# Performance work log

Measured on AMD Instinct MI355X. Metric: run time of the kernel, lower is better.

## Reference

```python
import jax, jax.numpy as jnp
import numpy as np

LAMBDA_DEPTHG = 0.3
STEGO_TEMPERATURE = 0.1
KNN_K = 7
DEPTH_SIGMA = 0.5
EPS = 1e-8


def _l2norm(x):
    return x / jnp.sqrt(jnp.sum(x * x, axis=-1, keepdims=True) + EPS)


def _stego_loss(codes, feats, temperature, knn_k):
    # Pairwise cosine similarity of DINO features -> KNN graph (includes self).
    f = _l2norm(feats)                                  # (B,N,Df)
    sim_f = jnp.einsum('bnd,bmd->bnm', f, f)            # (B,N,N)
    _, knn_idx = jax.lax.top_k(sim_f, knn_k)            # (B,N,k) int32
    # Temperature-scaled InfoNCE over code similarities; KNN entries are positives.
    c = _l2norm(codes)                                  # (B,N,Dc)
    logits = jnp.einsum('bnd,bmd->bnm', c, c) / temperature  # (B,N,N)
    logp = jax.nn.log_softmax(logits, axis=-1)          # (B,N,N)
    pos_logp = jnp.take_along_axis(logp, knn_idx, axis=-1)   # (B,N,k)
    return -jnp.mean(pos_logp)


def _depth_guided_correlation_loss(codes, depth, sigma_d):
    # Gaussian depth affinity: pixels at similar depth should have similar codes.
    dd = depth[:, :, None] - depth[:, None, :]          # (B,N,N)
    w = jnp.exp(-(dd * dd) / (2.0 * sigma_d * sigma_d)) # (B,N,N)
    c = _l2norm(codes)
    s = jnp.einsum('bnd,bmd->bnm', c, c)                # (B,N,N) cosine corr
    return jnp.mean(w * (1.0 - s))


def setup_inputs() -> dict:
    key = jax.random.key(0)
    k1, k2, k3 = jax.random.split(key, 3)
    B, N = 2, 4096
    semantic_codes = jax.random.normal(k1, (B, N, 90), dtype=jnp.float32)
    dino_features = jax.random.normal(k2, (B, N, 384), dtype=jnp.float32)
    depth = jax.random.uniform(k3, (B, N), dtype=jnp.float32)
    return {"semantic_codes": semantic_codes, "dino_features": dino_features, "depth": depth}


def reference(semantic_codes, dino_features, depth):
    l_stego = _stego_loss(semantic_codes, dino_features, STEGO_TEMPERATURE, KNN_K)
    l_depthg = _depth_guided_correlation_loss(semantic_codes, depth, DEPTH_SIGMA)
    total = l_stego + LAMBDA_DEPTHG * l_depthg
    return (l_stego, l_depthg, total)
```

## Files before the change

kernel.cpp:

```cpp
#include <hip/hip_runtime.h>
#include <math.h>

#define NPTS 4096

typedef __attribute__((ext_vector_type(8))) short bf16x8;
typedef __attribute__((ext_vector_type(16))) float f32x16;

#define KEEP(x) asm volatile("" : "+v"(x))

__device__ __forceinline__ f32x16 zero16() {
  f32x16 z;
#pragma unroll
  for (int i = 0; i < 16; ++i) z[i] = 0.f;
  return z;
}

__device__ __forceinline__ unsigned packkey(float x, int m) {
  unsigned u = __float_as_uint(x);
  unsigned key = u ^ ((unsigned)((int)u >> 31) | 0x80000000u);
  return (key & 0xFFFFF000u) | (unsigned)m;
}

__device__ __forceinline__ void cas7(unsigned v, unsigned* s) {
#pragma unroll
  for (int t = 0; t < 7; ++t) {
    const unsigned hi = s[t] >= v ? s[t] : v;
    const unsigned lo = s[t] >= v ? v : s[t];
    s[t] = hi;
    v = lo;
  }
}

__device__ __forceinline__ unsigned bf16pack(float a, float b) {
  unsigned ua = __float_as_uint(a); ua = (ua + 0x7FFFu + ((ua >> 16) & 1u)) >> 16;
  unsigned ub = __float_as_uint(b); ub = (ub + 0x7FFFu + ((ub >> 16) & 1u)) >> 16;
  return ua | (ub << 16);
}

__global__ __launch_bounds__(64) void norm_f(const float* __restrict__ feats,
                                             unsigned short* __restrict__ Fsw) {
  const int row = blockIdx.x;
  const int lane = threadIdx.x;
  const int b = row >> 12, mt = (row >> 5) & 127, rl = row & 31;

  const float* f = feats + (size_t)row * 384;
  float v[8];
  float ss = 0.f;
  if (lane < 48) {
    float4 p0 = *(const float4*)(f + lane * 8);
    float4 p1 = *(const float4*)(f + lane * 8 + 4);
    v[0] = p0.x; v[1] = p0.y; v[2] = p0.z; v[3] = p0.w;
    v[4] = p1.x; v[5] = p1.y; v[6] = p1.z; v[7] = p1.w;
#pragma unroll
    for (int e = 0; e < 8; ++e) ss = fmaf(v[e], v[e], ss);
  }
#pragma unroll
  for (int m = 1; m <= 32; m <<= 1) ss += __shfl_xor(ss, m, 64);
  const float inv = rsqrtf(ss + 1e-8f);
  if (lane < 48) {
    uint4 o;
    o.x = bf16pack(v[0] * inv, v[1] * inv);
    o.y = bf16pack(v[2] * inv, v[3] * inv);
    o.z = bf16pack(v[4] * inv, v[5] * inv);
    o.w = bf16pack(v[6] * inv, v[7] * inv);
    const int kc = lane >> 1, hs = lane & 1;
    *(uint4*)(Fsw + (((size_t)(b * 128 + mt) * 24 + kc) << 9) + (hs * 32 + rl) * 8) = o;
  }
}

__global__ __launch_bounds__(64) void norm_c(const float* __restrict__ codes,
                                             unsigned short* __restrict__ Csw,
                                             float* __restrict__ invc) {
  const int row = blockIdx.x;
  const int lane = threadIdx.x;
  const int b = row >> 12, mt = (row >> 5) & 127, rl = row & 31;

  const float* c = codes + (size_t)row * 90;
  float cv[8];
#pragma unroll
  for (int e = 0; e < 8; ++e) cv[e] = 0.f;
  if (lane < 11) {
    float4 p0 = *(const float4*)(c + lane * 8);
    float4 p1 = *(const float4*)(c + lane * 8 + 4);
    cv[0] = p0.x; cv[1] = p0.y; cv[2] = p0.z; cv[3] = p0.w;
    cv[4] = p1.x; cv[5] = p1.y; cv[6] = p1.z; cv[7] = p1.w;
  } else if (lane == 11) {
    cv[0] = c[88]; cv[1] = c[89];
  }
  float cs = 0.f;
#pragma unroll
  for (int e = 0; e < 8; ++e) cs = fmaf(cv[e], cv[e], cs);
#pragma unroll
  for (int m = 1; m <= 32; m <<= 1) cs += __shfl_xor(cs, m, 64);
  const float cinv = rsqrtf(cs + 1e-8f);
  if (lane < 12) {
    uint4 o;
    o.x = bf16pack(cv[0] * cinv, cv[1] * cinv);
    o.y = bf16pack(cv[2] * cinv, cv[3] * cinv);
    o.z = bf16pack(cv[4] * cinv, cv[5] * cinv);
    o.w = bf16pack(cv[6] * cinv, cv[7] * cinv);
    const int kc = lane >> 1, hs = lane & 1;
    *(uint4*)(Csw + (((size_t)(b * 128 + mt) * 6 + kc) << 9) + (hs * 32 + rl) * 8) = o;
  }
  if (lane == 0) invc[row] = cinv;
}

__global__ __launch_bounds__(256, 1) void knn_mfma(const unsigned short* __restrict__ Fsw,
                                                   unsigned* __restrict__ cand) {
  __shared__ unsigned ckey[4][32][7];
  const int g = blockIdx.x;
  const int b = g & 1;
  const int p = (g >> 1) & 3;
  const int qt = g >> 3;
  const int q0 = qt * 32;
  const int tid = threadIdx.x;
  const int w = tid >> 6;
  const int lane = tid & 63;
  const int lo = lane & 31, hi4 = (lane >> 5) * 4;
  const unsigned short* Fb = Fsw + (size_t)b * 128 * 24 * 512;

  bf16x8 bfr[24];
  {
    const unsigned short* qb = Fb + ((size_t)qt * 24) * 512 + lane * 8;
#pragma unroll
    for (int t = 0; t < 24; ++t) bfr[t] = *(const bf16x8*)(qb + t * 512);
#pragma unroll
    for (int t = 0; t < 24; ++t) KEEP(bfr[t]);
  }
  unsigned s7[7];
#pragma unroll
  for (int t = 0; t < 7; ++t) s7[t] = 0u;

  const int t0 = p * 32 + w * 8;
  const unsigned short* ab = Fb + ((size_t)t0 * 24) * 512 + lane * 8;

  bf16x8 a0[12], a1[12];
#pragma unroll
  for (int t = 0; t < 12; ++t) a0[t] = *(const bf16x8*)(ab + t * 512);
#pragma unroll
  for (int t = 0; t < 12; ++t) KEEP(a0[t]);

  for (int mt = 0; mt < 8; ++mt) {
    const unsigned short* art = ab + (size_t)mt * 24 * 512;
#pragma unroll
    for (int t = 0; t < 12; ++t) a1[t] = *(const bf16x8*)(art + (12 + t) * 512);
#pragma unroll
    for (int t = 0; t < 12; ++t) KEEP(a1[t]);
    f32x16 acc = zero16();
#pragma unroll
    for (int t = 0; t < 12; ++t)
      acc = __builtin_amdgcn_mfma_f32_32x32x16_bf16(a0[t], bfr[t], acc, 0, 0, 0);
    if (mt + 1 < 8) {
      const unsigned short* arn = ab + (size_t)(mt + 1) * 24 * 512;
#pragma unroll
      for (int t = 0; t < 12; ++t) a0[t] = *(const bf16x8*)(arn + t * 512);
#pragma unroll
      for (int t = 0; t < 12; ++t) KEEP(a0[t]);
    }
#pragma unroll
    for (int t = 0; t < 12; ++t)
      acc = __builtin_amdgcn_mfma_f32_32x32x16_bf16(a1[t], bfr[12 + t], acc, 0, 0, 0);
    const int mb = (t0 + mt) * 32 + hi4;
#pragma unroll
    for (int r = 0; r < 16; ++r) {
      const int m = mb + (r & 3) + 8 * (r >> 2);
      cas7(packkey(acc[r], m), s7);
    }
  }

#pragma unroll
  for (int t = 0; t < 7; ++t) {
    const unsigned ov = (unsigned)__shfl_xor((int)s7[t], 32, 64);
    cas7(ov, s7);
  }
  if (lane < 32) {
#pragma unroll
    for (int t = 0; t < 7; ++t) ckey[w][lo][t] = s7[t];
  }
  __syncthreads();

  if (tid < 32) {
    unsigned fs[7];
#pragma unroll
    for (int t = 0; t < 7; ++t) fs[t] = 0u;
    for (int w2 = 0; w2 < 4; ++w2)
#pragma unroll
      for (int t = 0; t < 7; ++t) cas7(ckey[w2][tid][t], fs);
    unsigned* o = cand + ((size_t)((p * 2 + b) * NPTS) + q0 + tid) * 7;
#pragma unroll
    for (int t = 0; t < 7; ++t) o[t] = fs[t];
  }
}

__global__ __launch_bounds__(256, 1) void lse_depth(const unsigned short* __restrict__ Csw,
                                                    const float* __restrict__ depth,
                                                    float* __restrict__ slse_part,
                                                    float* __restrict__ dpart) {
  __shared__ float lsep[4][32];
  __shared__ float depp[4];
  const int g = blockIdx.x;
  const int b = g & 1;
  const int p = (g >> 1) & 3;
  const int qt = g >> 3;
  const int q0 = qt * 32;
  const int tid = threadIdx.x;
  const int w = tid >> 6;
  const int lane = tid & 63;
  const int lo = lane & 31, hi4 = (lane >> 5) * 4;
  const unsigned short* Cb = Csw + (size_t)b * 128 * 6 * 512;
  const float* db = depth + b * NPTS;

  bf16x8 bfr[6];
  {
    const unsigned short* qb = Cb + ((size_t)qt * 6) * 512 + lane * 8;
#pragma unroll
    for (int t = 0; t < 6; ++t) bfr[t] = *(const bf16x8*)(qb + t * 512);
#pragma unroll
    for (int t = 0; t < 6; ++t) KEEP(bfr[t]);
  }
  const float dq = db[q0 + lo];
  float slse = 0.f, sdep = 0.f;

  const int t0 = p * 32 + w * 8;
  const unsigned short* ab = Cb + ((size_t)t0 * 6) * 512 + lane * 8;

  bf16x8 a0[6], a1[6];
#pragma unroll
  for (int t = 0; t < 6; ++t) a0[t] = *(const bf16x8*)(ab + t * 512);
#pragma unroll
  for (int t = 0; t < 6; ++t) KEEP(a0[t]);

#define PROC3(A, GT)                                                           \
  {                                                                            \
    f32x16 acc = zero16();                                                     \
    _Pragma("unroll")                                                          \
    for (int t = 0; t < 6; ++t)                                                \
      acc = __builtin_amdgcn_mfma_f32_32x32x16_bf16(A[t], bfr[t], acc, 0, 0, 0); \
    float dvv[16];                                                             \
    _Pragma("unroll")                                                          \
    for (int k = 0; k < 4; ++k) {                                              \
      float4 dv = *(const float4*)(db + (GT) * 32 + hi4 + 8 * k);              \
      dvv[k * 4 + 0] = dv.x; dvv[k * 4 + 1] = dv.y;                            \
      dvv[k * 4 + 2] = dv.z; dvv[k * 4 + 3] = dv.w;                            \
    }                                                                          \
    _Pragma("unroll")                                                          \
    for (int r = 0; r < 16; ++r) {                                             \
      const float s = acc[r];                                                  \
      const float dd = dq - dvv[r];                                            \
      sdep += __expf(-2.f * dd * dd) * (1.f - s);                              \
      slse += __expf(fmaf(s, 10.f, -10.f));                                    \
    }                                                                          \
  }

  for (int mt = 0; mt < 8; mt += 2) {
    {
      const unsigned short* ar = ab + (size_t)(mt + 1) * 6 * 512;
#pragma unroll
      for (int t = 0; t < 6; ++t) a1[t] = *(const bf16x8*)(ar + t * 512);
#pragma unroll
      for (int t = 0; t < 6; ++t) KEEP(a1[t]);
    }
    PROC3(a0, t0 + mt)
    if (mt + 2 < 8) {
      const unsigned short* ar = ab + (size_t)(mt + 2) * 6 * 512;
#pragma unroll
      for (int t = 0; t < 6; ++t) a0[t] = *(const bf16x8*)(ar + t * 512);
#pragma unroll
      for (int t = 0; t < 6; ++t) KEEP(a0[t]);
    }
    PROC3(a1, t0 + mt + 1)
  }
#undef PROC3

  slse += __shfl_xor(slse, 32, 64);
  if (lane < 32) lsep[w][lo] = slse;
#pragma unroll
  for (int m = 1; m <= 32; m <<= 1) sdep += __shfl_xor(sdep, m, 64);
  if (lane == 0) depp[w] = sdep;
  __syncthreads();
  if (tid < 32) {
    float tot = 0.f;
#pragma unroll
    for (int w2 = 0; w2 < 4; ++w2) tot += lsep[w2][tid];
    slse_part[(size_t)((p * 2 + b) * NPTS) + q0 + tid] = tot;
  }
  if (tid == 32) {
    float d = 0.f;
#pragma unroll
    for (int w2 = 0; w2 < 4; ++w2) d += depp[w2];
    dpart[g] = d;
  }
}

__global__ __launch_bounds__(64) void gather_pos(const float* __restrict__ codes,
                                                 const float* __restrict__ invc,
                                                 const unsigned* __restrict__ cand,
                                                 float* __restrict__ gpart) {
  const int n = blockIdx.x;
  const int b = n >> 12, q = n & 4095;
  const int lane = threadIdx.x;

  unsigned s[7];
#pragma unroll
  for (int t = 0; t < 7; ++t) s[t] = 0u;
#pragma unroll
  for (int pp = 0; pp < 4; ++pp) {
    const unsigned* cp = cand + ((size_t)((pp * 2 + b) * NPTS) + q) * 7;
#pragma unroll
    for (int t = 0; t < 7; ++t) cas7(cp[t], s);
  }
  bool has = false;
#pragma unroll
  for (int t = 0; t < 7; ++t) has = has || ((s[t] & 4095u) == (unsigned)q);
  if (!has) s[6] = (unsigned)q;

  const float* cn = codes + (size_t)n * 90;
  float2 a = make_float2(0.f, 0.f);
  if (lane < 45) a = *(const float2*)(cn + lane * 2);
  const float inva = invc[n];
  float ssum = 0.f;
#pragma unroll
  for (int k = 0; k < 7; ++k) {
    const int m = (int)(s[k] & 4095u);
    const float* cm = codes + ((size_t)(b << 12) + m) * 90;
    float2 bb = make_float2(0.f, 0.f);
    if (lane < 45) bb = *(const float2*)(cm + lane * 2);
    float p = fmaf(a.x, bb.x, a.y * bb.y);
#pragma unroll
    for (int w = 1; w <= 32; w <<= 1) p += __shfl_xor(p, w, 64);
    ssum += p * inva * invc[(b << 12) + m];
  }
  if (lane == 0) gpart[n] = ssum;
}

__global__ __launch_bounds__(256) void finalize(const float* __restrict__ slse_part,
                                                const float* __restrict__ gpart,
                                                const float* __restrict__ dpart,
                                                float* __restrict__ out) {
  const int tid = threadIdx.x;
  float s1 = 0.f, s2 = 0.f;
  for (int n = tid; n < 2 * NPTS; n += 256) {
    const int b = n >> 12, q = n & 4095;
    float pz = 0.f;
#pragma unroll
    for (int pp = 0; pp < 4; ++pp) pz += slse_part[(pp * 2 + b) * NPTS + q];
    s1 += 10.f + __logf(pz);
    s2 += gpart[n];
  }
  float s3 = 0.f;
#pragma unroll
  for (int k = 0; k < 4; ++k) s3 += dpart[tid + k * 256];
  __shared__ float r1[256], r2[256], r3[256];
  r1[tid] = s1; r2[tid] = s2; r3[tid] = s3;
  __syncthreads();
  for (int s = 128; s > 0; s >>= 1) {
    if (tid < s) { r1[tid] += r1[tid + s]; r2[tid] += r2[tid + s]; r3[tid] += r3[tid + s]; }
    __syncthreads();
  }
  if (tid == 0) {
    const float l_st = (7.f * r1[0] - 10.f * r2[0]) / 57344.f;
    const float l_dp = r3[0] / 33554432.f;
    out[0] = l_st;
    out[1] = l_dp;
    out[2] = l_st + 0.3f * l_dp;
  }
}

extern "C" void kernel_launch(void* const* d_in, const int* in_sizes, int n_in,
                              void* d_out, int out_size, void* d_ws, size_t ws_size,
                              hipStream_t stream) {
  (void)in_sizes; (void)n_in; (void)out_size; (void)ws_size;
  const float* codes = (const float*)d_in[0];
  const float* feats = (const float*)d_in[1];
  const float* depth = (const float*)d_in[2];
  float* out = (float*)d_out;

  char* ws = (char*)d_ws;
  float*    invc      = (float*)ws;
  unsigned* cand      = (unsigned*)(ws + 32768);
  unsigned short* Fsw = (unsigned short*)(ws + 950272);
  unsigned short* Csw = (unsigned short*)(ws + 950272);
  float*    slse_part = (float*)(ws + 2523136);
  float*    dpart     = (float*)(ws + 2654208);
  float*    gpart     = (float*)(ws + 2658304);

  norm_f<<<2 * NPTS, 64, 0, stream>>>(feats, Fsw);
  knn_mfma<<<1024, 256, 0, stream>>>(Fsw, cand);
  norm_c<<<2 * NPTS, 64, 0, stream>>>(codes, Csw, invc);
  lse_depth<<<1024, 256, 0, stream>>>(Csw, depth, slse_part, dpart);
  gather_pos<<<2 * NPTS, 64, 0, stream>>>(codes, invc, cand, gpart);
  finalize<<<1, 256, 0, stream>>>(slse_part, gpart, dpart, out);
}
```

Before: 101.8 us.

## Pipeline top-k epilogue with next tile MFMAs and skip insertions below threshold

The KNN candidate kernel now double-buffers accumulators, so the top-7 insertion for the previous 32x32 tile is interleaved with the MFMA chain of the current tile. Each candidate insertion is also gated by a wave-wide check against the current 7th-best key, which skips most of the sorting-network work. The sentinel initial key changes to a small finite value so the threshold can be unpacked as a float. This adds a wave vote per element and relies on divergence-free branches, and it raises register pressure from the second accumulator.

```diff
diff --git a/kernel.cpp b/kernel.cpp
--- a/kernel.cpp
+++ b/kernel.cpp
@@ -19,6 +19,11 @@
   unsigned u = __float_as_uint(x);
   unsigned key = u ^ ((unsigned)((int)u >> 31) | 0x80000000u);
   return (key & 0xFFFFF000u) | (unsigned)m;
+}
+
+__device__ __forceinline__ float unpackkey(unsigned key) {
+  const unsigned m1 = (unsigned)((int)key >> 31);
+  return __uint_as_float(key ^ ((~m1) | 0x80000000u));
 }
 
 __device__ __forceinline__ void cas7(unsigned v, unsigned* s) {
@@ -30,6 +35,8 @@
     v = lo;
   }
 }
+
+#define KSENT 0x00800000u
 
 __device__ __forceinline__ unsigned bf16pack(float a, float b) {
   unsigned ua = __float_as_uint(a); ua = (ua + 0x7FFFu + ((ua >> 16) & 1u)) >> 16;
@@ -129,44 +136,66 @@
   }
   unsigned s7[7];
 #pragma unroll
-  for (int t = 0; t < 7; ++t) s7[t] = 0u;
+  for (int t = 0; t < 7; ++t) s7[t] = KSENT;
 
   const int t0 = p * 32 + w * 8;
   const unsigned short* ab = Fb + ((size_t)t0 * 24) * 512 + lane * 8;
 
   bf16x8 a0[12], a1[12];
-#pragma unroll
-  for (int t = 0; t < 12; ++t) a0[t] = *(const bf16x8*)(ab + t * 512);
-#pragma unroll
-  for (int t = 0; t < 12; ++t) KEEP(a0[t]);
-
-  for (int mt = 0; mt < 8; ++mt) {
-    const unsigned short* art = ab + (size_t)mt * 24 * 512;
-#pragma unroll
-    for (int t = 0; t < 12; ++t) a1[t] = *(const bf16x8*)(art + (12 + t) * 512);
-#pragma unroll
-    for (int t = 0; t < 12; ++t) KEEP(a1[t]);
-    f32x16 acc = zero16();
-#pragma unroll
-    for (int t = 0; t < 12; ++t)
-      acc = __builtin_amdgcn_mfma_f32_32x32x16_bf16(a0[t], bfr[t], acc, 0, 0, 0);
-    if (mt + 1 < 8) {
-      const unsigned short* arn = ab + (size_t)(mt + 1) * 24 * 512;
-#pragma unroll
-      for (int t = 0; t < 12; ++t) a0[t] = *(const bf16x8*)(arn + t * 512);
-#pragma unroll
-      for (int t = 0; t < 12; ++t) KEEP(a0[t]);
-    }
-#pragma unroll
-    for (int t = 0; t < 12; ++t)
-      acc = __builtin_amdgcn_mfma_f32_32x32x16_bf16(a1[t], bfr[12 + t], acc, 0, 0, 0);
-    const int mb = (t0 + mt) * 32 + hi4;
-#pragma unroll
-    for (int r = 0; r < 16; ++r) {
-      const int m = mb + (r & 3) + 8 * (r >> 2);
-      cas7(packkey(acc[r], m), s7);
-    }
-  }
+
+#define LOADA0(MT)                                                             \
+  { const unsigned short* ar_ = ab + (size_t)(MT) * 24 * 512;                  \
+    _Pragma("unroll")                                                          \
+    for (int t = 0; t < 12; ++t) a0[t] = *(const bf16x8*)(ar_ + t * 512);      \
+    _Pragma("unroll")                                                          \
+    for (int t = 0; t < 12; ++t) KEEP(a0[t]); }
+
+#define LOADA1(MT)                                                             \
+  { const unsigned short* ar_ = ab + (size_t)(MT) * 24 * 512;                  \
+    _Pragma("unroll")                                                          \
+    for (int t = 0; t < 12; ++t) a1[t] = *(const bf16x8*)(ar_ + (12 + t) * 512); \
+    _Pragma("unroll")                                                          \
+    for (int t = 0; t < 12; ++t) KEEP(a1[t]); }
+
+#define EPI8(ACC, MT, R0)                                                      \
+  { const float thr_ = unpackkey(s7[6]);                                       \
+    const int mb_ = (t0 + (MT)) * 32 + hi4;                                    \
+    _Pragma("unroll")                                                          \
+    for (int r = (R0); r < (R0) + 8; ++r) {                                    \
+      const float v_ = ACC[r];                                                 \
+      if (__any(v_ > thr_))                                                    \
+        cas7(packkey(v_, mb_ + (r & 3) + 8 * (r >> 2)), s7);                   \
+    } }
+
+#define TILE(ACC, MT, PACC, PMT, DOEPI)                                        \
+  LOADA1(MT)                                                                   \
+  ACC = zero16();                                                              \
+  _Pragma("unroll")                                                            \
+  for (int t = 0; t < 12; ++t)                                                 \
+    ACC = __builtin_amdgcn_mfma_f32_32x32x16_bf16(a0[t], bfr[t], ACC, 0, 0, 0); \
+  if (DOEPI) { EPI8(PACC, PMT, 0) }                                            \
+  if ((MT) + 1 < 8) { LOADA0((MT) + 1) }                                       \
+  _Pragma("unroll")                                                            \
+  for (int t = 0; t < 12; ++t)                                                 \
+    ACC = __builtin_amdgcn_mfma_f32_32x32x16_bf16(a1[t], bfr[12 + t], ACC, 0, 0, 0); \
+  if (DOEPI) { EPI8(PACC, PMT, 8) }
+
+  LOADA0(0)
+  f32x16 accA, accB;
+  TILE(accA, 0, accB, 0, 0)
+  TILE(accB, 1, accA, 0, 1)
+  TILE(accA, 2, accB, 1, 1)
+  TILE(accB, 3, accA, 2, 1)
+  TILE(accA, 4, accB, 3, 1)
+  TILE(accB, 5, accA, 4, 1)
+  TILE(accA, 6, accB, 5, 1)
+  TILE(accB, 7, accA, 6, 1)
+  EPI8(accB, 7, 0)
+  EPI8(accB, 7, 8)
+#undef TILE
+#undef EPI8
+#undef LOADA0
+#undef LOADA1
 
 #pragma unroll
   for (int t = 0; t < 7; ++t) {
@@ -182,7 +211,7 @@
   if (tid < 32) {
     unsigned fs[7];
 #pragma unroll
-    for (int t = 0; t < 7; ++t) fs[t] = 0u;
+    for (int t = 0; t < 7; ++t) fs[t] = KSENT;
     for (int w2 = 0; w2 < 4; ++w2)
 #pragma unroll
       for (int t = 0; t < 7; ++t) cas7(ckey[w2][tid][t], fs);
@@ -302,7 +331,7 @@
 
   unsigned s[7];
 #pragma unroll
-  for (int t = 0; t < 7; ++t) s[t] = 0u;
+  for (int t = 0; t < 7; ++t) s[t] = KSENT;
 #pragma unroll
   for (int pp = 0; pp < 4; ++pp) {
     const unsigned* cp = cand + ((size_t)((pp * 2 + b) * NPTS) + q) * 7;
```

Result: slower. 130.2 us (+27.9%).

## Use FP8 MFMA for KNN similarity and widen lse_depth blocks to 512 threads

Applied to the files above, without the earlier changes.

Normalized DINO features are now stored as FP8 (scaled by 8) instead of bf16, and the KNN similarity GEMM uses the fp8 32x32x16 MFMA. This halves the feature bytes loaded and uses a higher-throughput MFMA path. The cost is lower precision in the similarity values, which could change which neighbours top-k selects. Separately, lse_depth switches to 512 blocks of 512 threads, so the workspace keeps two partial sums instead of four and finalize reduces fewer partials.

```diff
diff --git a/kernel.cpp b/kernel.cpp
--- a/kernel.cpp
+++ b/kernel.cpp
@@ -5,6 +5,7 @@
 
 typedef __attribute__((ext_vector_type(8))) short bf16x8;
 typedef __attribute__((ext_vector_type(16))) float f32x16;
+typedef long fp8x8;
 
 #define KEEP(x) asm volatile("" : "+v"(x))
 
@@ -31,6 +32,8 @@
   }
 }
 
+#define KSENT 0u
+
 __device__ __forceinline__ unsigned bf16pack(float a, float b) {
   unsigned ua = __float_as_uint(a); ua = (ua + 0x7FFFu + ((ua >> 16) & 1u)) >> 16;
   unsigned ub = __float_as_uint(b); ub = (ub + 0x7FFFu + ((ub >> 16) & 1u)) >> 16;
@@ -38,7 +41,7 @@
 }
 
 __global__ __launch_bounds__(64) void norm_f(const float* __restrict__ feats,
-                                             unsigned short* __restrict__ Fsw) {
+                                             unsigned char* __restrict__ Fsw8) {
   const int row = blockIdx.x;
   const int lane = threadIdx.x;
   const int b = row >> 12, mt = (row >> 5) & 127, rl = row & 31;
@@ -56,15 +59,15 @@
   }
 #pragma unroll
   for (int m = 1; m <= 32; m <<= 1) ss += __shfl_xor(ss, m, 64);
-  const float inv = rsqrtf(ss + 1e-8f);
+  const float s8 = rsqrtf(ss + 1e-8f) * 8.0f;
   if (lane < 48) {
-    uint4 o;
-    o.x = bf16pack(v[0] * inv, v[1] * inv);
-    o.y = bf16pack(v[2] * inv, v[3] * inv);
-    o.z = bf16pack(v[4] * inv, v[5] * inv);
-    o.w = bf16pack(v[6] * inv, v[7] * inv);
+    int w0 = __builtin_amdgcn_cvt_pk_fp8_f32(v[0] * s8, v[1] * s8, 0, 0);
+    w0 = __builtin_amdgcn_cvt_pk_fp8_f32(v[2] * s8, v[3] * s8, w0, 1);
+    int w1 = __builtin_amdgcn_cvt_pk_fp8_f32(v[4] * s8, v[5] * s8, 0, 0);
+    w1 = __builtin_amdgcn_cvt_pk_fp8_f32(v[6] * s8, v[7] * s8, w1, 1);
     const int kc = lane >> 1, hs = lane & 1;
-    *(uint4*)(Fsw + (((size_t)(b * 128 + mt) * 24 + kc) << 9) + (hs * 32 + rl) * 8) = o;
+    uint2 o = make_uint2((unsigned)w0, (unsigned)w1);
+    *(uint2*)(Fsw8 + (((size_t)(b * 128 + mt) * 24 + kc) << 9) + (hs * 32 + rl) * 8) = o;
   }
 }
 
@@ -105,7 +108,7 @@
   if (lane == 0) invc[row] = cinv;
 }
 
-__global__ __launch_bounds__(256, 1) void knn_mfma(const unsigned short* __restrict__ Fsw,
+__global__ __launch_bounds__(256, 1) void knn_mfma(const unsigned char* __restrict__ Fsw8,
                                                    unsigned* __restrict__ cand) {
   __shared__ unsigned ckey[4][32][7];
   const int g = blockIdx.x;
@@ -117,49 +120,49 @@
   const int w = tid >> 6;
   const int lane = tid & 63;
   const int lo = lane & 31, hi4 = (lane >> 5) * 4;
-  const unsigned short* Fb = Fsw + (size_t)b * 128 * 24 * 512;
-
-  bf16x8 bfr[24];
+  const unsigned char* Fb = Fsw8 + (size_t)b * 128 * 24 * 512;
+
+  fp8x8 bfr[24];
   {
-    const unsigned short* qb = Fb + ((size_t)qt * 24) * 512 + lane * 8;
-#pragma unroll
-    for (int t = 0; t < 24; ++t) bfr[t] = *(const bf16x8*)(qb + t * 512);
+    const unsigned char* qb = Fb + ((size_t)qt * 24) * 512 + lane * 8;
+#pragma unroll
+    for (int t = 0; t < 24; ++t) bfr[t] = *(const fp8x8*)(qb + t * 512);
 #pragma unroll
     for (int t = 0; t < 24; ++t) KEEP(bfr[t]);
   }
   unsigned s7[7];
 #pragma unroll
-  for (int t = 0; t < 7; ++t) s7[t] = 0u;
+  for (int t = 0; t < 7; ++t) s7[t] = KSENT;
 
   const int t0 = p * 32 + w * 8;
-  const unsigned short* ab = Fb + ((size_t)t0 * 24) * 512 + lane * 8;
-
-  bf16x8 a0[12], a1[12];
-#pragma unroll
-  for (int t = 0; t < 12; ++t) a0[t] = *(const bf16x8*)(ab + t * 512);
+  const unsigned char* ab = Fb + ((size_t)t0 * 24) * 512 + lane * 8;
+
+  fp8x8 a0[12], a1[12];
+#pragma unroll
+  for (int t = 0; t < 12; ++t) a0[t] = *(const fp8x8*)(ab + t * 512);
 #pragma unroll
   for (int t = 0; t < 12; ++t) KEEP(a0[t]);
 
   for (int mt = 0; mt < 8; ++mt) {
-    const unsigned short* art = ab + (size_t)mt * 24 * 512;
-#pragma unroll
-    for (int t = 0; t < 12; ++t) a1[t] = *(const bf16x8*)(art + (12 + t) * 512);
+    const unsigned char* art = ab + (size_t)mt * 24 * 512;
+#pragma unroll
+    for (int t = 0; t < 12; ++t) a1[t] = *(const fp8x8*)(art + (12 + t) * 512);
 #pragma unroll
     for (int t = 0; t < 12; ++t) KEEP(a1[t]);
     f32x16 acc = zero16();
 #pragma unroll
     for (int t = 0; t < 12; ++t)
-      acc = __builtin_amdgcn_mfma_f32_32x32x16_bf16(a0[t], bfr[t], acc, 0, 0, 0);
+      acc = __builtin_amdgcn_mfma_f32_32x32x16_fp8_fp8(a0[t], bfr[t], acc, 0, 0, 0);
     if (mt + 1 < 8) {
-      const unsigned short* arn = ab + (size_t)(mt + 1) * 24 * 512;
-#pragma unroll
-      for (int t = 0; t < 12; ++t) a0[t] = *(const bf16x8*)(arn + t * 512);
+      const unsigned char* arn = ab + (size_t)(mt + 1) * 24 * 512;
+#pragma unroll
+      for (int t = 0; t < 12; ++t) a0[t] = *(const fp8x8*)(arn + t * 512);
 #pragma unroll
       for (int t = 0; t < 12; ++t) KEEP(a0[t]);
     }
 #pragma unroll
     for (int t = 0; t < 12; ++t)
-      acc = __builtin_amdgcn_mfma_f32_32x32x16_bf16(a1[t], bfr[12 + t], acc, 0, 0, 0);
+      acc = __builtin_amdgcn_mfma_f32_32x32x16_fp8_fp8(a1[t], bfr[12 + t], acc, 0, 0, 0);
     const int mb = (t0 + mt) * 32 + hi4;
 #pragma unroll
     for (int r = 0; r < 16; ++r) {
@@ -182,7 +185,7 @@
   if (tid < 32) {
     unsigned fs[7];
 #pragma unroll
-    for (int t = 0; t < 7; ++t) fs[t] = 0u;
+    for (int t = 0; t < 7; ++t) fs[t] = KSENT;
     for (int w2 = 0; w2 < 4; ++w2)
 #pragma unroll
       for (int t = 0; t < 7; ++t) cas7(ckey[w2][tid][t], fs);
@@ -192,16 +195,16 @@
   }
 }
 
-__global__ __launch_bounds__(256, 1) void lse_depth(const unsigned short* __restrict__ Csw,
+__global__ __launch_bounds__(512, 1) void lse_depth(const unsigned short* __restrict__ Csw,
                                                     const float* __restrict__ depth,
                                                     float* __restrict__ slse_part,
                                                     float* __restrict__ dpart) {
-  __shared__ float lsep[4][32];
-  __shared__ float depp[4];
+  __shared__ float lsep[8][32];
+  __shared__ float depp[8];
   const int g = blockIdx.x;
   const int b = g & 1;
-  const int p = (g >> 1) & 3;
-  const int qt = g >> 3;
+  const int h = (g >> 1) & 1;
+  const int qt = g >> 2;
   const int q0 = qt * 32;
   const int tid = threadIdx.x;
   const int w = tid >> 6;
@@ -221,7 +224,7 @@
   const float dq = db[q0 + lo];
   float slse = 0.f, sdep = 0.f;
 
-  const int t0 = p * 32 + w * 8;
+  const int t0 = h * 64 + w * 8;
   const unsigned short* ab = Cb + ((size_t)t0 * 6) * 512 + lane * 8;
 
   bf16x8 a0[6], a1[6];
@@ -281,13 +284,13 @@
   if (tid < 32) {
     float tot = 0.f;
 #pragma unroll
-    for (int w2 = 0; w2 < 4; ++w2) tot += lsep[w2][tid];
-    slse_part[(size_t)((p * 2 + b) * NPTS) + q0 + tid] = tot;
+    for (int w2 = 0; w2 < 8; ++w2) tot += lsep[w2][tid];
+    slse_part[(size_t)((h * 2 + b) * NPTS) + q0 + tid] = tot;
   }
   if (tid == 32) {
     float d = 0.f;
 #pragma unroll
-    for (int w2 = 0; w2 < 4; ++w2) d += depp[w2];
+    for (int w2 = 0; w2 < 8; ++w2) d += depp[w2];
     dpart[g] = d;
   }
 }
@@ -302,7 +305,7 @@
 
   unsigned s[7];
 #pragma unroll
-  for (int t = 0; t < 7; ++t) s[t] = 0u;
+  for (int t = 0; t < 7; ++t) s[t] = KSENT;
 #pragma unroll
   for (int pp = 0; pp < 4; ++pp) {
     const unsigned* cp = cand + ((size_t)((pp * 2 + b) * NPTS) + q) * 7;
@@ -341,15 +344,11 @@
   float s1 = 0.f, s2 = 0.f;
   for (int n = tid; n < 2 * NPTS; n += 256) {
     const int b = n >> 12, q = n & 4095;
-    float pz = 0.f;
-#pragma unroll
-    for (int pp = 0; pp < 4; ++pp) pz += slse_part[(pp * 2 + b) * NPTS + q];
+    const float pz = slse_part[b * NPTS + q] + slse_part[(2 + b) * NPTS + q];
     s1 += 10.f + __logf(pz);
     s2 += gpart[n];
   }
-  float s3 = 0.f;
-#pragma unroll
-  for (int k = 0; k < 4; ++k) s3 += dpart[tid + k * 256];
+  float s3 = dpart[tid] + dpart[tid + 256];
   __shared__ float r1[256], r2[256], r3[256];
   r1[tid] = s1; r2[tid] = s2; r3[tid] = s3;
   __syncthreads();
@@ -378,16 +377,16 @@
   char* ws = (char*)d_ws;
   float*    invc      = (float*)ws;
   unsigned* cand      = (unsigned*)(ws + 32768);
-  unsigned short* Fsw = (unsigned short*)(ws + 950272);
-  unsigned short* Csw = (unsigned short*)(ws + 950272);
+  unsigned char*  Fsw8 = (unsigned char*)(ws + 950272);
+  unsigned short* Csw  = (unsigned short*)(ws + 950272);
   float*    slse_part = (float*)(ws + 2523136);
   float*    dpart     = (float*)(ws + 2654208);
   float*    gpart     = (float*)(ws + 2658304);
 
-  norm_f<<<2 * NPTS, 64, 0, stream>>>(feats, Fsw);
-  knn_mfma<<<1024, 256, 0, stream>>>(Fsw, cand);
+  norm_f<<<2 * NPTS, 64, 0, stream>>>(feats, Fsw8);
+  knn_mfma<<<1024, 256, 0, stream>>>(Fsw8, cand);
   norm_c<<<2 * NPTS, 64, 0, stream>>>(codes, Csw, invc);
-  lse_depth<<<1024, 256, 0, stream>>>(Csw, depth, slse_part, dpart);
+  lse_depth<<<512, 512, 0, stream>>>(Csw, depth, slse_part, dpart);
   gather_pos<<<2 * NPTS, 64, 0, stream>>>(codes, invc, cand, gpart);
   finalize<<<1, 256, 0, stream>>>(slse_part, gpart, dpart, out);
 }
```

Result: faster. 92.65 us (-9.0%).
